# Performance work log

Measured on AMD Instinct MI355X. Metric: run time of the kernel, lower is better.

The kernel has to match this reference:

```python
import jax, jax.numpy as jnp
import numpy as np

# Model dims (match init_kwargs)
D_MODEL = 2048
H = 16        # query heads
HKV = 4       # kv heads (GQA)
DS = 32       # semantic head dim (compressed)
DG = 32       # geometric head dim (compressed, RoPE'd)
DV = 64       # value head dim
B, T = 2, 4096
MB = 64       # mem_block
LW = 1024     # local_window
ROPE_BASE = 10000.0
NEG_INF = -1e9


def _rope(x, pos, base):
    # x: [B, h, T, d] with d even; standard rotate-half RoPE
    d = x.shape[-1]
    inv_freq = 1.0 / (base ** (jnp.arange(0, d, 2, dtype=jnp.float32) / d))
    ang = pos.astype(jnp.float32)[:, None] * inv_freq          # [T, d/2]
    cos, sin = jnp.cos(ang), jnp.sin(ang)                      # [T, d/2]
    x1, x2 = jnp.split(x, 2, axis=-1)
    return jnp.concatenate([x1 * cos - x2 * sin,
                            x2 * cos + x1 * sin], axis=-1)


def setup_inputs() -> dict:
    key = jax.random.key(0)
    ks = jax.random.split(key, 8)
    w = lambda k, sh: jax.random.normal(k, sh, jnp.float32) * 0.02
    return {
        "x": jax.random.normal(ks[0], (B, T, D_MODEL), jnp.float32),
        "Wq_sem": w(ks[1], (D_MODEL, H * DS)),
        "Wk_sem": w(ks[2], (D_MODEL, HKV * DS)),
        "Wq_geo": w(ks[3], (D_MODEL, H * DG)),
        "Wk_geo": w(ks[4], (D_MODEL, HKV * DG)),
        "Wv": w(ks[5], (D_MODEL, HKV * DV)),
        "Wo": w(ks[6], (H * DV, D_MODEL)),
        "logit_scale": jnp.zeros((H,), jnp.float32),
    }


def reference(x, Wq_sem, Wk_sem, Wq_geo, Wk_geo, Wv, Wo, logit_scale):
    Bq, Tq = x.shape[0], x.shape[1]
    split = lambda y, h, d: y.reshape(Bq, Tq, h, d).transpose(0, 2, 1, 3)
    # Decoupled projections
    q_sem = split(x @ Wq_sem, H, DS)      # [B,H,T,DS]
    k_sem = split(x @ Wk_sem, HKV, DS)    # [B,HKV,T,DS]
    q_geo = split(x @ Wq_geo, H, DG)
    k_geo = split(x @ Wk_geo, HKV, DG)
    v = split(x @ Wv, HKV, DV)            # [B,HKV,T,DV]
    pos = jnp.arange(Tq)
    # RoPE only on the geometric path
    q_geo = _rope(q_geo, pos, ROPE_BASE)
    k_geo = _rope(k_geo, pos, ROPE_BASE)
    # Memory-block summarization: mean-pool remote KV into one token per block
    remote = Tq - LW
    nblk = remote // MB
    pool = lambda a: jnp.concatenate(
        [a[:, :, :remote].reshape(Bq, HKV, nblk, MB, a.shape[-1]).mean(axis=3),
         a[:, :, remote:]], axis=2)
    k_sem2, k_geo2, v2 = pool(k_sem), pool(k_geo), pool(v)  # [B,HKV,K,*], K=nblk+LW
    k_pos = jnp.concatenate([jnp.arange(nblk) * MB + (MB - 1),
                             jnp.arange(remote, Tq)])        # [K]
    # GQA head-group broadcast
    rep = lambda a: jnp.repeat(a, H // HKV, axis=1)
    k_sem2, k_geo2, v2 = rep(k_sem2), rep(k_geo2), rep(v2)   # [B,H,K,*]
    # Decoupled scores: semantic + geometric, each with its own scale
    scores = (jnp.einsum('bhqd,bhkd->bhqk', q_sem, k_sem2) * (1.0 / jnp.sqrt(float(DS)))
              + jnp.einsum('bhqd,bhkd->bhqk', q_geo, k_geo2) * (1.0 / jnp.sqrt(float(DG))))
    # Learned per-head temperature
    scores = scores * jnp.exp(logit_scale)[None, :, None, None]
    # Causal mask over summarized key positions
    mask = k_pos[None, :] <= pos[:, None]                    # [T,K]
    scores = jnp.where(mask[None, None], scores, NEG_INF)
    probs = jax.nn.softmax(scores, axis=-1)
    out = jnp.einsum('bhqk,bhkd->bhqd', probs, v2)           # [B,H,T,DV]
    out = out.transpose(0, 2, 1, 3).reshape(Bq, Tq, H * DV)
    return out @ Wo                                          # [B,T,D_MODEL]
```

## Files before the change

### kernel.cpp

```cpp
#include <hip/hip_runtime.h>
#include <math.h>

#define B_  2
#define T_  4096
#define DM  2048
#define H_  16
#define HKV 4
#define DV_ 64
#define MB_ 64
#define LW_ 1024
#define REMOTE 3072
#define NBLK 48
#define KTOT 1072
#define NTILES 17

typedef __bf16 bf16x8 __attribute__((ext_vector_type(8)));
typedef float  f32x4  __attribute__((ext_vector_type(4)));

__device__ __forceinline__ float bf2f(unsigned short u) {
    unsigned int x = ((unsigned int)u) << 16;
    return __builtin_bit_cast(float, x);
}
__device__ __forceinline__ unsigned short f2bf(float f) {
    unsigned int x = __builtin_bit_cast(unsigned int, f);
    x = x + 0x7fffu + ((x >> 16) & 1u);
    return (unsigned short)(x >> 16);
}

__device__ __forceinline__ void gload16(const unsigned short* gsrc,
                                        unsigned short* ldst) {
    __builtin_amdgcn_global_load_lds(
        (const __attribute__((address_space(1))) void*)gsrc,
        (__attribute__((address_space(3))) void*)ldst,
        16, 0, 0);
}

__global__ void cvt_f32_to_bf16(const float* __restrict__ src,
                                unsigned short* __restrict__ dst, int n) {
    int i = (blockIdx.x * blockDim.x + threadIdx.x) * 4;
    if (i >= n) return;
    float4 v = *(const float4*)(src + i);
    ushort4 o;
    o.x = f2bf(v.x); o.y = f2bf(v.y); o.z = f2bf(v.z); o.w = f2bf(v.w);
    *(ushort4*)(dst + i) = o;
}

__global__ void transpose_cvt(const float* __restrict__ src,
                              unsigned short* __restrict__ dst, int R, int C) {
    __shared__ float tile[32][33];
    int ct = blockIdx.x, rt = blockIdx.y;
    int tx = threadIdx.x, ty = threadIdx.y;
    #pragma unroll
    for (int i = ty; i < 32; i += 8)
        tile[i][tx] = src[(size_t)(rt * 32 + i) * C + ct * 32 + tx];
    __syncthreads();
    #pragma unroll
    for (int i = ty; i < 32; i += 8)
        dst[(size_t)(ct * 32 + i) * R + rt * 32 + tx] = f2bf(tile[tx][i]);
}

template<int MODE>
__global__ __launch_bounds__(256, 3) void gemmP(
    const unsigned short* __restrict__ A,
    const unsigned short* __restrict__ BT,
    float* __restrict__ outF,
    unsigned short* __restrict__ qcat,
    unsigned short* __restrict__ kp,
    unsigned short* __restrict__ vt,
    int M, int N, int K, int nbx)
{
    extern __shared__ __align__(16) unsigned short lds[];

    const int tid = threadIdx.x;
    const int lane = tid & 63, w = tid >> 6;
    const int wr = w >> 1, wc = w & 1;
    const int l15 = lane & 15, lg = lane >> 4;

    const int cpx = gridDim.x >> 3;
    const int swz = (blockIdx.x & 7) * cpx + (blockIdx.x >> 3);
    const int bx = swz % nbx, by = swz / nbx;
    const int row0 = by * 128, col0 = bx * 128;

    const int scol = ((lane & 3) ^ ((lane >> 3) & 3)) * 8;
    const int srA = w * 16 + (lane >> 2);
    const unsigned short* Ag = A  + (size_t)row0 * K;
    const unsigned short* Bg = BT + (size_t)col0 * K;

    const int rdsw = (lg ^ ((l15 >> 1) & 3)) * 8;
    const int aoff = (wr * 64 + l15) * 32 + rdsw;
    const int boff = (wc * 64 + l15) * 32 + rdsw;

    const int NT = K >> 5;
    f32x4 acc[4][4] = {};

    auto stage = [&](int s, int kk) {
        unsigned short* sa = lds + s * 8192;
        unsigned short* sb = sa + 4096;
        #pragma unroll
        for (int j = 0; j < 2; j++) {
            gload16(Ag + (size_t)(srA + j * 64) * K + kk + scol,
                    sa + (j * 256 + w * 64) * 8);
            gload16(Bg + (size_t)(srA + j * 64) * K + kk + scol,
                    sb + (j * 256 + w * 64) * 8);
        }
    };

    stage(0, 0);
    stage(1, 32);
    asm volatile("s_waitcnt vmcnt(4)" ::: "memory");

    int rs = 0;
    for (int t = 0; t < NT; ++t) {
        __builtin_amdgcn_s_barrier();
        const bool st = (t + 2) < NT;
        if (st) stage(rs == 0 ? 2 : rs - 1, (t + 2) << 5);

        const unsigned short* As_ = lds + rs * 8192;
        const unsigned short* Bs_ = As_ + 4096;
        bf16x8 af[4], bfr[4];
        #pragma unroll
        for (int mf = 0; mf < 4; mf++)
            af[mf] = __builtin_bit_cast(bf16x8, *(const uint4*)&As_[aoff + mf * 512]);
        #pragma unroll
        for (int nf = 0; nf < 4; nf++)
            bfr[nf] = __builtin_bit_cast(bf16x8, *(const uint4*)&Bs_[boff + nf * 512]);

        __builtin_amdgcn_s_setprio(1);
        #pragma unroll
        for (int mf = 0; mf < 4; mf++)
            #pragma unroll
            for (int nf = 0; nf < 4; nf++)
                acc[mf][nf] = __builtin_amdgcn_mfma_f32_16x16x32_bf16(
                                  af[mf], bfr[nf], acc[mf][nf], 0, 0, 0);
        __builtin_amdgcn_s_setprio(0);

        if (st) asm volatile("s_waitcnt vmcnt(4)" ::: "memory");
        else    asm volatile("s_waitcnt vmcnt(0)" ::: "memory");
        rs = (rs == 2) ? 0 : rs + 1;
    }

    if (MODE == 1) {
        #pragma unroll
        for (int mf = 0; mf < 4; mf++)
            #pragma unroll
            for (int nf = 0; nf < 4; nf++)
                #pragma unroll
                for (int r = 0; r < 4; r++) {
                    int row = row0 + wr * 64 + mf * 16 + lg * 4 + r;
                    int col = col0 + wc * 64 + nf * 16 + l15;
                    outF[(size_t)row * N + col] = acc[mf][nf][r];
                }
    } else {
        const int cspan = col0 + wc * 64;
        const int tbase = row0 & 4095;
        const int bq = row0 >> 12;

        if ((cspan >= 512 && cspan < 1024) || (cspan >= 1152 && cspan < 1280)) {
            const float invf = exp2f(-(float)l15 * 0.8304820237218406f);
            #pragma unroll
            for (int mf = 0; mf < 4; mf++) {
                #pragma unroll
                for (int r = 0; r < 4; r++) {
                    float s, c;
                    sincosf((float)(tbase + wr*64 + mf*16 + lg*4 + r) * invf, &s, &c);
                    float a0 = acc[mf][0][r], a1 = acc[mf][1][r];
                    acc[mf][0][r] = a0 * c - a1 * s;
                    acc[mf][1][r] = a1 * c + a0 * s;
                    float a2 = acc[mf][2][r], a3 = acc[mf][3][r];
                    acc[mf][2][r] = a2 * c - a3 * s;
                    acc[mf][3][r] = a3 * c + a2 * s;
                }
            }
        }

        if (cspan < 1024) {
            #pragma unroll
            for (int nf = 0; nf < 4; nf++) {
                int col = cspan + nf * 16 + l15;
                int h = (col < 512) ? (col >> 5) : ((col - 512) >> 5);
                int d = (col < 512) ? (col & 31) : (32 + (col & 31));
                unsigned short* qb =
                    qcat + (((size_t)(bq * 16 + h)) * 4096 + tbase) * 64 + d;
                #pragma unroll
                for (int mf = 0; mf < 4; mf++)
                    #pragma unroll
                    for (int r = 0; r < 4; r++)
                        qb[(size_t)(wr*64 + mf*16 + lg*4 + r) * 64] =
                            f2bf(acc[mf][nf][r]);
            }
        } else if (tbase >= REMOTE) {
            #pragma unroll
            for (int nf = 0; nf < 4; nf++) {
                int col = cspan + nf * 16 + l15;
                #pragma unroll
                for (int mf = 0; mf < 4; mf++)
                    #pragma unroll
                    for (int r = 0; r < 4; r++) {
                        int key = tbase + wr*64 + mf*16 + lg*4 + r - 3024;
                        unsigned short hv = f2bf(acc[mf][nf][r]);
                        if (col < 1280) {
                            int g, dk;
                            if (col < 1152) { g = (col - 1024) >> 5; dk = col & 31; }
                            else            { g = (col - 1152) >> 5; dk = 32 + (col & 31); }
                            kp[(((size_t)(bq*4 + g)) * KTOT + key) * 64 + dk] = hv;
                        } else {
                            int g = (col - 1280) >> 6, dv = col & 63;
                            vt[(((size_t)(bq*4 + g)) * 64 + dv) * KTOT + key] = hv;
                        }
                    }
            }
        } else {
            #pragma unroll
            for (int nf = 0; nf < 4; nf++) {
                float ps = 0.f;
                #pragma unroll
                for (int mf = 0; mf < 4; mf++)
                    #pragma unroll
                    for (int r = 0; r < 4; r++) ps += acc[mf][nf][r];
                ps += __shfl_xor(ps, 16);
                ps += __shfl_xor(ps, 32);
                if (lane < 16) {
                    int col = cspan + nf * 16 + l15;
                    int key = (tbase >> 6) + wr;
                    unsigned short hv = f2bf(ps * (1.f / 64.f));
                    if (col < 1280) {
                        int g, dk;
                        if (col < 1152) { g = (col - 1024) >> 5; dk = col & 31; }
                        else            { g = (col - 1152) >> 5; dk = 32 + (col & 31); }
                        kp[(((size_t)(bq*4 + g)) * KTOT + key) * 64 + dk] = hv;
                    } else {
                        int g = (col - 1280) >> 6, dv = col & 63;
                        vt[(((size_t)(bq*4 + g)) * 64 + dv) * KTOT + key] = hv;
                    }
                }
            }
        }
    }
}

__global__ __launch_bounds__(256) void attn_fwd(
    const unsigned short* __restrict__ qcat,
    const unsigned short* __restrict__ kp,
    const unsigned short* __restrict__ vt,
    const float* __restrict__ ls,
    unsigned short* __restrict__ attn_out)
{
    __shared__ unsigned short Pl[4][32][72];

    const int tid = threadIdx.x;
    const int lane = tid & 63, w = tid >> 6;
    const int l15 = lane & 15, lg = lane >> 4;

    const int wid = blockIdx.x * 4 + w;
    const int hb = wid & 31;
    const int iu = wid >> 5;
    int i;
    if (iu < 32)       i = 127 - iu;
    else if (iu == 32) i = 0;
    else if (iu == 33) i = 1;
    else               i = iu - 32;
    const int h = hb & 15, b = hb >> 4, g = h >> 2;
    const int q0 = i * 32;

    int ktmax;
    if (q0 < 64) ktmax = NTILES;
    else {
        int lastkey = q0 + 31 - 3024;
        ktmax = (lastkey < NBLK) ? 1 : (lastkey / 64 + 1);
    }

    const float sc = __expf(ls[h]) * 0.17677669529663687f;

    bf16x8 aq[2][2];
    const unsigned short* qbase = qcat + (((size_t)(b * 16 + h)) * T_ + q0) * 64;
    #pragma unroll
    for (int rf = 0; rf < 2; rf++)
        #pragma unroll
        for (int kh = 0; kh < 2; kh++)
            aq[rf][kh] = __builtin_bit_cast(bf16x8,
                *(const uint4*)(qbase + (size_t)(rf*16 + l15)*64 + kh*32 + lg*8));

    float m[2][4], lrun[2][4];
    #pragma unroll
    for (int rf = 0; rf < 2; rf++)
        #pragma unroll
        for (int r = 0; r < 4; r++) { m[rf][r] = -1e9f; lrun[rf][r] = 0.f; }
    f32x4 oacc[2][4] = {};

    const unsigned short* kbase = kp + ((size_t)(b * 4 + g)) * KTOT * 64;
    const unsigned short* vbase = vt + ((size_t)(b * 4 + g)) * 64 * KTOT;

    for (int kt = 0; kt < ktmax; kt++) {
        const int kb = kt * 64;

        bf16x8 bk[4][2];
        #pragma unroll
        for (int nf = 0; nf < 4; nf++) {
            int krow = kb + nf*16 + l15;
            int krc = krow < KTOT ? krow : KTOT - 1;
            #pragma unroll
            for (int kh = 0; kh < 2; kh++)
                bk[nf][kh] = __builtin_bit_cast(bf16x8,
                    *(const uint4*)(kbase + (size_t)krc * 64 + kh*32 + lg*8));
        }

        f32x4 s[2][4] = {};
        #pragma unroll
        for (int rf = 0; rf < 2; rf++)
            #pragma unroll
            for (int nf = 0; nf < 4; nf++)
                #pragma unroll
                for (int kh = 0; kh < 2; kh++)
                    s[rf][nf] = __builtin_amdgcn_mfma_f32_16x16x32_bf16(
                                    aq[rf][kh], bk[nf][kh], s[rf][nf], 0, 0, 0);

        bf16x8 bv[4][2];
        #pragma unroll
        for (int nfv = 0; nfv < 4; nfv++)
            #pragma unroll
            for (int kh = 0; kh < 2; kh++) {
                int kc = kb + kh*32 + lg*8;
                int kcc = (kc + 8 <= KTOT) ? kc : KTOT - 8;
                bv[nfv][kh] = __builtin_bit_cast(bf16x8,
                    *(const uint4*)(vbase + (size_t)(nfv*16 + l15) * KTOT + kcc));
            }

        #pragma unroll
        for (int rf = 0; rf < 2; rf++) {
            #pragma unroll
            for (int r = 0; r < 4; r++) {
                const int qpos = q0 + rf*16 + lg*4 + r;
                float vals[4];
                float tmax = -INFINITY;
                #pragma unroll
                for (int nf = 0; nf < 4; nf++) {
                    int key = kb + nf*16 + l15;
                    float v = s[rf][nf][r] * sc;
                    int kpos = (key < NBLK) ? key * 64 + 63 : 3024 + key;
                    v = (key < KTOT) ? ((kpos <= qpos) ? v : -1e9f) : -INFINITY;
                    vals[nf] = v;
                    tmax = fmaxf(tmax, v);
                }
                #pragma unroll
                for (int d = 1; d < 16; d <<= 1)
                    tmax = fmaxf(tmax, __shfl_xor(tmax, d));
                float mn = fmaxf(m[rf][r], tmax);
                float scl = __expf(m[rf][r] - mn);
                m[rf][r] = mn;
                float rs = 0.f;
                #pragma unroll
                for (int nf = 0; nf < 4; nf++) {
                    unsigned short pb = f2bf(__expf(vals[nf] - mn));
                    rs += bf2f(pb);
                    Pl[w][rf*16 + lg*4 + r][nf*16 + l15] = pb;
                }
                #pragma unroll
                for (int d = 1; d < 16; d <<= 1)
                    rs += __shfl_xor(rs, d);
                lrun[rf][r] = lrun[rf][r] * scl + rs;
                #pragma unroll
                for (int nfv = 0; nfv < 4; nfv++)
                    oacc[rf][nfv][r] *= scl;
            }
        }

        #pragma unroll
        for (int rf = 0; rf < 2; rf++) {
            bf16x8 pa[2];
            #pragma unroll
            for (int kh = 0; kh < 2; kh++)
                pa[kh] = __builtin_bit_cast(bf16x8,
                    *(const uint4*)&Pl[w][rf*16 + l15][kh*32 + lg*8]);
            #pragma unroll
            for (int nfv = 0; nfv < 4; nfv++)
                #pragma unroll
                for (int kh = 0; kh < 2; kh++)
                    oacc[rf][nfv] = __builtin_amdgcn_mfma_f32_16x16x32_bf16(
                                        pa[kh], bv[nfv][kh], oacc[rf][nfv], 0, 0, 0);
        }
    }

    #pragma unroll
    for (int rf = 0; rf < 2; rf++) {
        #pragma unroll
        for (int r = 0; r < 4; r++) {
            float inv = 1.f / lrun[rf][r];
            int q = q0 + rf*16 + lg*4 + r;
            size_t obase = ((size_t)(b * T_ + q)) * 1024 + h * 64;
            #pragma unroll
            for (int nfv = 0; nfv < 4; nfv++)
                attn_out[obase + nfv*16 + l15] = f2bf(oacc[rf][nfv][r] * inv);
        }
    }
}

extern "C" void kernel_launch(void* const* d_in, const int* in_sizes, int n_in,
                              void* d_out, int out_size, void* d_ws, size_t ws_size,
                              hipStream_t stream) {
    const float* x      = (const float*)d_in[0];
    const float* Wq_sem = (const float*)d_in[1];
    const float* Wk_sem = (const float*)d_in[2];
    const float* Wq_geo = (const float*)d_in[3];
    const float* Wk_geo = (const float*)d_in[4];
    const float* Wv     = (const float*)d_in[5];
    const float* Wo     = (const float*)d_in[6];
    const float* ls     = (const float*)d_in[7];

    char* w = (char*)d_ws;
    auto alloc = [&](size_t bytes) {
        char* p = w;
        w += (bytes + 255) & ~(size_t)255;
        return p;
    };
    unsigned short* xb    = (unsigned short*)alloc((size_t)8192 * 2048 * 2);
    unsigned short* WcatT = (unsigned short*)alloc((size_t)1536 * 2048 * 2);
    unsigned short* WoT   = (unsigned short*)alloc((size_t)2048 * 1024 * 2);
    unsigned short* qcat  = (unsigned short*)alloc((size_t)2 * 16 * 4096 * 64 * 2);
    unsigned short* kp    = (unsigned short*)alloc((size_t)2 * 4 * 1072 * 64 * 2);
    unsigned short* vt    = (unsigned short*)alloc((size_t)2 * 4 * 1072 * 64 * 2);
    unsigned short* aout  = (unsigned short*)alloc((size_t)8192 * 1024 * 2);

    hipFuncSetAttribute(reinterpret_cast<const void*>(&gemmP<0>),
                        hipFuncAttributeMaxDynamicSharedMemorySize, 49152);
    hipFuncSetAttribute(reinterpret_cast<const void*>(&gemmP<1>),
                        hipFuncAttributeMaxDynamicSharedMemorySize, 49152);

    cvt_f32_to_bf16<<<16384, 256, 0, stream>>>(x, xb, 8192 * 2048);

    dim3 tb(32, 8);
    transpose_cvt<<<dim3(16, 64), tb, 0, stream>>>(Wq_sem, WcatT + (size_t)0    * 2048, 2048, 512);
    transpose_cvt<<<dim3(16, 64), tb, 0, stream>>>(Wq_geo, WcatT + (size_t)512  * 2048, 2048, 512);
    transpose_cvt<<<dim3( 4, 64), tb, 0, stream>>>(Wk_sem, WcatT + (size_t)1024 * 2048, 2048, 128);
    transpose_cvt<<<dim3( 4, 64), tb, 0, stream>>>(Wk_geo, WcatT + (size_t)1152 * 2048, 2048, 128);
    transpose_cvt<<<dim3( 8, 64), tb, 0, stream>>>(Wv,     WcatT + (size_t)1280 * 2048, 2048, 256);
    transpose_cvt<<<dim3(64, 32), tb, 0, stream>>>(Wo, WoT, 1024, 2048);

    gemmP<0><<<768, 256, 49152, stream>>>(
        xb, WcatT, nullptr, qcat, kp, vt, 8192, 1536, 2048, 12);

    attn_fwd<<<dim3(1024), 256, 0, stream>>>(qcat, kp, vt, ls, aout);

    gemmP<1><<<1024, 256, 49152, stream>>>(
        aout, WoT, (float*)d_out, nullptr, nullptr, nullptr, 8192, 2048, 1024, 16);
}
```

Before: 203.4 us.

## Merge weight transposes into one launch and shrink output GEMM LDS ring

The six weight transpose-convert launches become a single kernel that picks its source matrix from the block index. The x conversion kernel now uses a grid-stride loop over 2048 blocks instead of one float4 per thread. The output-projection GEMM switches from a 3-stage to a 2-stage LDS ring (32KB) with launch bounds raised to 4 blocks per CU, trading prefetch depth for occupancy.

```diff
diff --git a/kernel.cpp b/kernel.cpp
--- a/kernel.cpp
+++ b/kernel.cpp
@@ -36,20 +36,34 @@
 }
 
 __global__ void cvt_f32_to_bf16(const float* __restrict__ src,
-                                unsigned short* __restrict__ dst, int n) {
-    int i = (blockIdx.x * blockDim.x + threadIdx.x) * 4;
-    if (i >= n) return;
-    float4 v = *(const float4*)(src + i);
-    ushort4 o;
-    o.x = f2bf(v.x); o.y = f2bf(v.y); o.z = f2bf(v.z); o.w = f2bf(v.w);
-    *(ushort4*)(dst + i) = o;
-}
-
-__global__ void transpose_cvt(const float* __restrict__ src,
-                              unsigned short* __restrict__ dst, int R, int C) {
+                                unsigned short* __restrict__ dst, int n4) {
+    int stride = gridDim.x * blockDim.x;
+    for (int i = blockIdx.x * blockDim.x + threadIdx.x; i < n4; i += stride) {
+        float4 v = ((const float4*)src)[i];
+        ushort4 o = make_ushort4(f2bf(v.x), f2bf(v.y), f2bf(v.z), f2bf(v.w));
+        ((ushort4*)dst)[i] = o;
+    }
+}
+
+__global__ void transpose_all(const float* __restrict__ Wq_sem,
+                              const float* __restrict__ Wq_geo,
+                              const float* __restrict__ Wk_sem,
+                              const float* __restrict__ Wk_geo,
+                              const float* __restrict__ Wv,
+                              const float* __restrict__ Wo,
+                              unsigned short* __restrict__ WcatT,
+                              unsigned short* __restrict__ WoT) {
     __shared__ float tile[32][33];
-    int ct = blockIdx.x, rt = blockIdx.y;
-    int tx = threadIdx.x, ty = threadIdx.y;
+    const int bid = blockIdx.x;
+    const float* src; unsigned short* dst; int R, C, tiles_x, lt;
+    if (bid < 1024)      { src = Wq_sem; dst = WcatT;                       R = 2048; C = 512;  tiles_x = 16; lt = bid; }
+    else if (bid < 2048) { src = Wq_geo; dst = WcatT + (size_t)512  * 2048; R = 2048; C = 512;  tiles_x = 16; lt = bid - 1024; }
+    else if (bid < 2304) { src = Wk_sem; dst = WcatT + (size_t)1024 * 2048; R = 2048; C = 128;  tiles_x = 4;  lt = bid - 2048; }
+    else if (bid < 2560) { src = Wk_geo; dst = WcatT + (size_t)1152 * 2048; R = 2048; C = 128;  tiles_x = 4;  lt = bid - 2304; }
+    else if (bid < 3072) { src = Wv;     dst = WcatT + (size_t)1280 * 2048; R = 2048; C = 256;  tiles_x = 8;  lt = bid - 2560; }
+    else                 { src = Wo;     dst = WoT;                         R = 1024; C = 2048; tiles_x = 64; lt = bid - 3072; }
+    const int ct = lt % tiles_x, rt = lt / tiles_x;
+    const int tx = threadIdx.x, ty = threadIdx.y;
     #pragma unroll
     for (int i = ty; i < 32; i += 8)
         tile[i][tx] = src[(size_t)(rt * 32 + i) * C + ct * 32 + tx];
@@ -60,7 +74,7 @@
 }
 
 template<int MODE>
-__global__ __launch_bounds__(256, 3) void gemmP(
+__global__ __launch_bounds__(256, MODE == 1 ? 4 : 3) void gemmP(
     const unsigned short* __restrict__ A,
     const unsigned short* __restrict__ BT,
     float* __restrict__ outF,
@@ -69,6 +83,7 @@
     unsigned short* __restrict__ vt,
     int M, int N, int K, int nbx)
 {
+    constexpr int RING = (MODE == 1) ? 2 : 3;
     extern __shared__ __align__(16) unsigned short lds[];
 
     const int tid = threadIdx.x;
@@ -105,15 +120,23 @@
         }
     };
 
-    stage(0, 0);
-    stage(1, 32);
-    asm volatile("s_waitcnt vmcnt(4)" ::: "memory");
+    if (RING == 3) {
+        stage(0, 0);
+        stage(1, 32);
+        asm volatile("s_waitcnt vmcnt(4)" ::: "memory");
+    } else {
+        stage(0, 0);
+        asm volatile("s_waitcnt vmcnt(0)" ::: "memory");
+    }
 
     int rs = 0;
     for (int t = 0; t < NT; ++t) {
         __builtin_amdgcn_s_barrier();
-        const bool st = (t + 2) < NT;
-        if (st) stage(rs == 0 ? 2 : rs - 1, (t + 2) << 5);
+        if (RING == 3) {
+            if (t + 2 < NT) stage(rs == 0 ? 2 : rs - 1, (t + 2) << 5);
+        } else {
+            if (t + 1 < NT) stage(rs ^ 1, (t + 1) << 5);
+        }
 
         const unsigned short* As_ = lds + rs * 8192;
         const unsigned short* Bs_ = As_ + 4096;
@@ -134,9 +157,14 @@
                                   af[mf], bfr[nf], acc[mf][nf], 0, 0, 0);
         __builtin_amdgcn_s_setprio(0);
 
-        if (st) asm volatile("s_waitcnt vmcnt(4)" ::: "memory");
-        else    asm volatile("s_waitcnt vmcnt(0)" ::: "memory");
-        rs = (rs == 2) ? 0 : rs + 1;
+        if (RING == 3) {
+            if (t + 2 < NT) asm volatile("s_waitcnt vmcnt(4)" ::: "memory");
+            else            asm volatile("s_waitcnt vmcnt(0)" ::: "memory");
+            rs = (rs == 2) ? 0 : rs + 1;
+        } else {
+            if (t + 1 < NT) asm volatile("s_waitcnt vmcnt(0)" ::: "memory");
+            rs ^= 1;
+        }
     }
 
     if (MODE == 1) {
@@ -423,23 +451,18 @@
     hipFuncSetAttribute(reinterpret_cast<const void*>(&gemmP<0>),
                         hipFuncAttributeMaxDynamicSharedMemorySize, 49152);
     hipFuncSetAttribute(reinterpret_cast<const void*>(&gemmP<1>),
-                        hipFuncAttributeMaxDynamicSharedMemorySize, 49152);
-
-    cvt_f32_to_bf16<<<16384, 256, 0, stream>>>(x, xb, 8192 * 2048);
-
-    dim3 tb(32, 8);
-    transpose_cvt<<<dim3(16, 64), tb, 0, stream>>>(Wq_sem, WcatT + (size_t)0    * 2048, 2048, 512);
-    transpose_cvt<<<dim3(16, 64), tb, 0, stream>>>(Wq_geo, WcatT + (size_t)512  * 2048, 2048, 512);
-    transpose_cvt<<<dim3( 4, 64), tb, 0, stream>>>(Wk_sem, WcatT + (size_t)1024 * 2048, 2048, 128);
-    transpose_cvt<<<dim3( 4, 64), tb, 0, stream>>>(Wk_geo, WcatT + (size_t)1152 * 2048, 2048, 128);
-    transpose_cvt<<<dim3( 8, 64), tb, 0, stream>>>(Wv,     WcatT + (size_t)1280 * 2048, 2048, 256);
-    transpose_cvt<<<dim3(64, 32), tb, 0, stream>>>(Wo, WoT, 1024, 2048);
+                        hipFuncAttributeMaxDynamicSharedMemorySize, 32768);
+
+    cvt_f32_to_bf16<<<2048, 256, 0, stream>>>(x, xb, 8192 * 2048 / 4);
+
+    transpose_all<<<5120, dim3(32, 8), 0, stream>>>(
+        Wq_sem, Wq_geo, Wk_sem, Wk_geo, Wv, Wo, WcatT, WoT);
 
     gemmP<0><<<768, 256, 49152, stream>>>(
         xb, WcatT, nullptr, qcat, kp, vt, 8192, 1536, 2048, 12);
 
     attn_fwd<<<dim3(1024), 256, 0, stream>>>(qcat, kp, vt, ls, aout);
 
-    gemmP<1><<<1024, 256, 49152, stream>>>(
+    gemmP<1><<<1024, 256, 32768, stream>>>(
         aout, WoT, (float*)d_out, nullptr, nullptr, nullptr, 8192, 2048, 1024, 16);
 }
```

After: 193.5 us. 1.05x faster.
